# Performance work log

Measured on AMD Instinct MI355X. Metric: run time of the kernel, lower is better.

Reference implementation:

```python
import jax, jax.numpy as jnp
import numpy as np

N, C, T, V = 32, 64, 256, 25   # batch, channels, frames, joints
REL, OUT, K = 8, 64, 5         # rel_channels = C//8, out_channels, 5 topology branches
NU = 17                        # upper-body joints (lower = V - NU = 8)


def setup_inputs() -> dict:
    key = jax.random.key(0)
    ks = jax.random.split(key, 8)
    sC = np.float32(1.0 / np.sqrt(C))
    sR = np.float32(1.0 / np.sqrt(REL))
    return {
        "x": jax.random.normal(ks[0], (N, C, T, V), jnp.float32),
        "A": jax.random.uniform(ks[1], (K, V, V), jnp.float32),
        # stacked 1x1-conv weights for the 5 branches (conv{k}_1_1, _1_2, _2, _3, _4)
        "W11": jax.random.normal(ks[2], (K, REL, C), jnp.float32) * sC,
        "b11": jnp.zeros((K, REL), jnp.float32),
        "W12": jax.random.normal(ks[3], (K, REL, C), jnp.float32) * sC,
        "b12": jnp.zeros((K, REL), jnp.float32),
        "W2": jax.random.normal(ks[4], (K, REL, C), jnp.float32) * sC,
        "b2": jnp.zeros((K, REL), jnp.float32),
        "W3": jax.random.normal(ks[5], (K, OUT, C), jnp.float32) * sC,
        "b3": jnp.zeros((K, OUT), jnp.float32),
        "W4": jax.random.normal(ks[6], (K, OUT, REL), jnp.float32) * sR,
        "b4": jnp.zeros((K, OUT), jnp.float32),
    }


def reference(x, A, W11, b11, W12, b12, W2, b2, W3, b3, W4, b4):
    # 1x1 conv followed by mean over T commutes with the (linear) conv:
    # conv(x).mean(T) == W @ x.mean(T) + b. Pool once, reuse across branches.
    mu = jnp.mean(x[:, :, :, :NU], axis=2)   # (N, C, 17)
    ml = jnp.mean(x[:, :, :, NU:], axis=2)   # (N, C, 8)

    u11 = jnp.einsum('krc,ncv->knrv', W11, mu) + b11[:, None, :, None]  # (K,N,R,17)
    u2 = jnp.einsum('krc,ncv->knrv', W2, mu) + b2[:, None, :, None]     # (K,N,R,17)
    l12 = jnp.einsum('krc,ncv->knrv', W12, ml) + b12[:, None, :, None]  # (K,N,R,8)
    l2 = jnp.einsum('krc,ncv->knrv', W2, ml) + b2[:, None, :, None]     # (K,N,R,8)

    # pairwise-difference topology blocks
    x_a = jnp.tanh(u11[..., :, None] - u2[..., None, :])   # (K,N,R,17,17)
    x_b = jnp.tanh(u11[..., :, None] - l2[..., None, :])   # (K,N,R,17,8)
    x_c = jnp.tanh(l12[..., :, None] - u2[..., None, :])   # (K,N,R,8,17)
    x_d = jnp.tanh(l12[..., :, None] - l2[..., None, :])   # (K,N,R,8,8)

    up = jnp.concatenate([x_a, x_b], axis=-1)   # (K,N,R,17,25)
    lo = jnp.concatenate([x_c, x_d], axis=-1)   # (K,N,R,8,25)

    # the original rotates the upper blocks: branch k uses upper from branch (k+1)%5
    up_rot = jnp.concatenate([up[1:], up[:1]], axis=0)
    full = jnp.concatenate([up_rot, lo], axis=-2)  # (K,N,R,25,25)

    graphs = jnp.einsum('kor,knruv->knouv', W4, full) + b4[:, None, :, None, None]  # (K,N,O,25,25)

    alpha = jnp.ones((K,), jnp.float32)  # default branch scales
    g = graphs * alpha[:, None, None, None, None] + A[:, None, None, :, :]

    x2 = jnp.einsum('koc,nctv->knotv', W3, x) + b3[:, None, :, None, None]  # (K,N,O,T,25)
    out = jnp.einsum('knouv,knotv->notu', g, x2)  # summed over the 5 branches
    return out, graphs
```

## Files before the change

### kernel.cpp

```cpp
#include <hip/hip_runtime.h>
#include <cstdint>
#include <cstddef>

#define N_  32
#define C_  64
#define T_  256
#define V_  25
#define R_  8
#define O_  64
#define K_  5
#define NU_ 17
#define U_  25
#define CV  (C_ * V_)
#define OG  2
#define NB  (OG * 32)

#define OUT_ELEMS ((size_t)N_ * O_ * T_ * V_)

typedef __attribute__((ext_vector_type(8))) short bf16x8;
typedef __attribute__((ext_vector_type(4))) float f32x4;

static __device__ __forceinline__ unsigned short f2bf(float f) {
    union { float f; unsigned u; } c; c.f = f;
    return (unsigned short)((c.u + 0x8000u) >> 16);
}
static __device__ __forceinline__ float bf2f(unsigned short h) {
    union { unsigned u; float f; } c; c.u = ((unsigned)h) << 16; return c.f;
}
static __device__ __forceinline__ float bf_lo(unsigned d) {
    union { unsigned u; float f; } c; c.u = d << 16; return c.f;
}
static __device__ __forceinline__ float bf_hi(unsigned d) {
    union { unsigned u; float f; } c; c.u = d & 0xFFFF0000u; return c.f;
}
static __device__ __forceinline__ unsigned pk2(float a, float b) {
    union { float f; unsigned u; } ca, cb; ca.f = a; cb.f = b;
    return ((ca.u + 0x8000u) >> 16) | ((cb.u + 0x8000u) & 0xFFFF0000u);
}
static __device__ __forceinline__ unsigned cvtpk(float a, float b) {
    unsigned r;
    asm("v_cvt_pk_bf16_f32 %0, %1, %2" : "=v"(r) : "v"(a), "v"(b));
    return r;
}

__global__ void k_xcast(const float* __restrict__ x, unsigned short* __restrict__ xT3,
                        float* __restrict__ pp) {
    __shared__ unsigned short tile[C_][408];
    int bid = blockIdx.x;
    int n = bid >> 4, tb = bid & 15;
    int tid = threadIdx.x;
    const float* xb = x + (size_t)n * C_ * T_ * V_ + tb * 400;
#pragma unroll
    for (int it = 0; it < 25; ++it) {
        int i = it * 256 + tid;
        int c = i / 100, q = i - c * 100;
        float4 v4 = *(const float4*)(xb + (size_t)c * (T_ * V_) + q * 4);
        uint2 w;
        w.x = pk2(v4.x, v4.y);
        w.y = pk2(v4.z, v4.w);
        *(uint2*)&tile[c][q * 4] = w;
    }
    __syncthreads();
    unsigned short* dstb = xT3 + ((size_t)(n * 16 + tb) * 200) * 128;
    for (int i = tid; i < 200 * 16; i += 256) {
        int sp = i >> 4, tl = i & 15;
        int v = sp >> 3, c0 = (sp & 7) * 8;
        unsigned short h[8];
#pragma unroll
        for (int j = 0; j < 8; ++j) h[j] = tile[c0 + j][tl * 25 + v];
        uint4 pk;
        pk.x = (unsigned)h[0] | ((unsigned)h[1] << 16);
        pk.y = (unsigned)h[2] | ((unsigned)h[3] << 16);
        pk.z = (unsigned)h[4] | ((unsigned)h[5] << 16);
        pk.w = (unsigned)h[6] | ((unsigned)h[7] << 16);
        *(uint4*)(dstb + (size_t)sp * 128 + tl * 8) = pk;
    }
    float* ppd = pp + ((size_t)n * 16 + tb) * CV;
    for (int e = tid; e < CV; e += 256) {
        int c = e / 25, v = e - c * 25;
        float s = 0.f;
#pragma unroll
        for (int t = 0; t < 16; ++t) s += bf2f(tile[c][t * 25 + v]);
        ppd[e] = s;
    }
}

__global__ void k_pool(const float* __restrict__ x, float* __restrict__ pool) {
    int nc = blockIdx.x;
    int t  = threadIdx.x;
    const float* px = x + ((size_t)nc * T_ + t) * V_;
    float acc[V_];
#pragma unroll
    for (int v = 0; v < V_; ++v) acc[v] = px[v];
#pragma unroll
    for (int off = 32; off > 0; off >>= 1) {
#pragma unroll
        for (int v = 0; v < V_; ++v) acc[v] += __shfl_down(acc[v], off, 64);
    }
    __shared__ float sm[4][V_];
    int wave = t >> 6, lane = t & 63;
    if (lane == 0) {
#pragma unroll
        for (int v = 0; v < V_; ++v) sm[wave][v] = acc[v];
    }
    __syncthreads();
    if (t < V_) {
        float s = sm[0][t] + sm[1][t] + sm[2][t] + sm[3][t];
        pool[(size_t)nc * V_ + t] = s * (1.0f / T_);
    }
}

__global__ void k_tvals(const float* __restrict__ pool,
                        const float* __restrict__ W11, const float* __restrict__ b11,
                        const float* __restrict__ W12, const float* __restrict__ b12,
                        const float* __restrict__ W2,  const float* __restrict__ b2,
                        float* __restrict__ t2o, float* __restrict__ tSo) {
    int kn = blockIdx.x;
    int k = kn / N_, n = kn % N_;
    int tid = threadIdx.x;
    int r = tid >> 5, v = tid & 31;
    if (v >= V_) return;
    const float* pp = pool + (size_t)n * C_ * V_ + v;
    const float* w2 = W2 + ((size_t)k * R_ + r) * C_;
    const float* w1 = ((v < NU_) ? W11 : W12) + ((size_t)k * R_ + r) * C_;
    float a2 = b2[k * R_ + r];
    float a1 = (v < NU_) ? b11[k * R_ + r] : b12[k * R_ + r];
    for (int c = 0; c < C_; ++c) {
        float p = pp[(size_t)c * V_];
        a2 += w2[c] * p;
        a1 += w1[c] * p;
    }
    size_t idx = (((size_t)k * N_ + n) * R_ + r) * V_ + v;
    t2o[idx] = a2;
    tSo[idx] = a1;
}

__global__ void k_graphs(const float* __restrict__ t2v, const float* __restrict__ tSv,
                         const float* __restrict__ W4, const float* __restrict__ b4,
                         float* __restrict__ graphs) {
    int kn = blockIdx.x;
    int k = kn / N_, n = kn % N_;
    int kup = (k + 1) % K_;
    __shared__ float F[R_][V_ * V_];
    __shared__ float w4s[O_][R_];
    __shared__ float b4s[O_];
    int tid = threadIdx.x;
    for (int i = tid; i < O_ * R_; i += 256) w4s[i / R_][i % R_] = W4[(size_t)k * O_ * R_ + i];
    if (tid < O_) b4s[tid] = b4[k * O_ + tid];
    for (int idx = tid; idx < R_ * V_ * V_; idx += 256) {
        int r = idx / (V_ * V_), uv = idx % (V_ * V_);
        int u = uv / V_, v = uv % V_;
        int ks = (u < NU_) ? kup : k;
        size_t base = (((size_t)ks * N_ + n) * R_ + r) * V_;
        F[r][uv] = tanhf(tSv[base + u] - t2v[base + v]);
    }
    __syncthreads();
    float* gout = graphs + ((size_t)k * N_ + n) * O_ * (V_ * V_);
    for (int idx = tid; idx < O_ * V_ * V_; idx += 256) {
        int o = idx / (V_ * V_), uv = idx % (V_ * V_);
        float a = b4s[o];
#pragma unroll
        for (int r = 0; r < R_; ++r) a += w4s[o][r] * F[r][uv];
        gout[idx] = a;
    }
}

__global__ void k_graphs2c(const float* __restrict__ pp,
                           const float* __restrict__ W11, const float* __restrict__ b11,
                           const float* __restrict__ W12, const float* __restrict__ b12,
                           const float* __restrict__ W2,  const float* __restrict__ b2,
                           const float* __restrict__ W4,  const float* __restrict__ b4,
                           float* __restrict__ graphs) {
    int bid = blockIdx.x;
    int og = bid & 1;
    int kn = bid >> 1;
    int k = kn / N_, n = kn % N_;
    int kup = (k + 1) % K_;
    __shared__ float poolL[CV];
    __shared__ float t2s[2][R_][V_];
    __shared__ float tSs[2][R_][V_];
    __shared__ float F[R_][V_ * V_];
    __shared__ float w4s[O_][R_];
    __shared__ float b4s[O_];
    int tid = threadIdx.x;
    for (int i = tid; i < O_ * R_; i += 512) w4s[i / R_][i % R_] = W4[(size_t)k * O_ * R_ + i];
    if (tid < O_) b4s[tid] = b4[k * O_ + tid];
    const float* ppn = pp + (size_t)n * 16 * CV;
    for (int i = tid; i < CV; i += 512) {
        float s = 0.f;
#pragma unroll
        for (int tb = 0; tb < 16; ++tb) s += ppn[(size_t)tb * CV + i];
        poolL[i] = s * (1.0f / T_);
    }
    __syncthreads();
    for (int i = tid; i < 2 * R_ * V_; i += 512) {
        int ks = i / (R_ * V_);
        int rem = i - ks * (R_ * V_);
        int r = rem / V_, v = rem - r * V_;
        int kk = ks ? kup : k;
        const float* w2 = W2 + ((size_t)kk * R_ + r) * C_;
        const float* w1 = ((v < NU_) ? W11 : W12) + ((size_t)kk * R_ + r) * C_;
        float a2 = b2[kk * R_ + r];
        float a1 = (v < NU_) ? b11[kk * R_ + r] : b12[kk * R_ + r];
        for (int c = 0; c < C_; ++c) {
            float p = poolL[c * 25 + v];
            a2 += w2[c] * p;
            a1 += w1[c] * p;
        }
        t2s[ks][r][v] = a2;
        tSs[ks][r][v] = a1;
    }
    __syncthreads();
    for (int idx = tid; idx < R_ * V_ * V_; idx += 512) {
        int r = idx / (V_ * V_), uv = idx % (V_ * V_);
        int u = uv / V_, v = uv % V_;
        int ks = (u < NU_) ? 1 : 0;
        F[r][uv] = tanhf(tSs[ks][r][u] - t2s[ks][r][v]);
    }
    __syncthreads();
    float* gout = graphs + ((size_t)k * N_ + n) * O_ * (V_ * V_);
    const int half = O_ * V_ * V_ / 2;
    for (int idx = og * half + tid; idx < (og + 1) * half; idx += 512) {
        int o = idx / (V_ * V_), uv = idx % (V_ * V_);
        float a = b4s[o];
#pragma unroll
        for (int r = 0; r < R_; ++r) a += w4s[o][r] * F[r][uv];
        gout[idx] = a;
    }
}

__global__ __launch_bounds__(256, 4) void k_main_fast(
    const unsigned short* __restrict__ xT3,
    const float* __restrict__ graphs,
    const float* __restrict__ Adj,
    const float* __restrict__ W3,
    const float* __restrict__ b3,
    float* __restrict__ out) {

    __shared__ unsigned short Hs[2][4][NB][8];
    __shared__ f32x4 Gls4[OG * 625];
    __shared__ float Gls1[OG * 625];
    __shared__ unsigned short W3kmh[K_ * OG * C_];
    __shared__ float biasS[NB];

    const int tid = threadIdx.x;
    int bid = blockIdx.x;
    bid = (bid & 7) * 128 + (bid >> 3);
    const int obase = (bid & 31) * OG;
    const int n = bid >> 5;
    const int lane = tid & 63;
    const int wv_ = tid >> 6;

    const size_t kstride = (size_t)N_ * O_ * 625;
    for (int i = tid; i < OG * 625; i += 256) {
        int o = i / 625, uv = i - o * 625;
        int u = uv / 25, v = uv - u * 25;
        size_t gb = ((size_t)n * O_ + obase + o) * 625 + uv;
        f32x4 g4;
        g4[0] = graphs[gb]               + Adj[uv];
        g4[1] = graphs[gb + kstride]     + Adj[625 + uv];
        g4[2] = graphs[gb + 2 * kstride] + Adj[1250 + uv];
        g4[3] = graphs[gb + 3 * kstride] + Adj[1875 + uv];
        int idx = o * 625 + v * 25 + u;
        Gls4[idx] = g4;
        Gls1[idx] = graphs[gb + 4 * kstride] + Adj[2500 + uv];
    }
    for (int i = tid; i < K_ * OG * C_; i += 256) {
        int k = i / (OG * C_);
        int rem = i - k * (OG * C_);
        int o = rem >> 6, c = rem & 63;
        W3kmh[(k * OG + o) * C_ + c] = f2bf(W3[((size_t)k * O_ + obase + o) * C_ + c]);
    }
    __syncthreads();

    if (tid < NB) {
        int o = tid >> 5, u = tid & 31;
        float bv = 0.f;
        if (u < U_) {
            f32x4 s4 = {0.f, 0.f, 0.f, 0.f};
            float s5 = 0.f;
            for (int v = 0; v < V_; ++v) {
                int idx = o * 625 + v * 25 + u;
                s4 += Gls4[idx];
                s5 += Gls1[idx];
            }
            bv = s4[0] * b3[0 * O_ + obase + o] + s4[1] * b3[1 * O_ + obase + o]
               + s4[2] * b3[2 * O_ + obase + o] + s4[3] * b3[3 * O_ + obase + o]
               + s5 * b3[4 * O_ + obase + o];
        }
        biasS[tid] = bv;
    }

    const int sl = wv_;
    const int hncol = lane;
    const int ho = hncol >> 5;
    const int hu = hncol & 31;
    const f32x4* gp4 = &Gls4[ho * 625 + hu];
    const float* gp1 = &Gls1[ho * 625 + hu];
    const unsigned short* wbh = &W3kmh[ho * C_ + sl * 8];
    uint4* hw = (uint4*)&Hs[0][sl][hncol][0];

    auto h_form = [&](uint4* hwp, const int parOff , f32x4 g, float g5) {
        float gk[5] = {g[0], g[1], g[2], g[3], g5};
        float h0 = 0.f, h1 = 0.f, h2 = 0.f, h3 = 0.f;
        float h4 = 0.f, h5 = 0.f, h6 = 0.f, h7 = 0.f;
#pragma unroll
        for (int k = 0; k < K_; ++k) {
            uint4 wk = *(const uint4*)(wbh + parOff + k * (OG * C_));
            float gv_ = gk[k];
            h0 += bf_lo(wk.x) * gv_; h1 += bf_hi(wk.x) * gv_;
            h2 += bf_lo(wk.y) * gv_; h3 += bf_hi(wk.y) * gv_;
            h4 += bf_lo(wk.z) * gv_; h5 += bf_hi(wk.z) * gv_;
            h6 += bf_lo(wk.w) * gv_; h7 += bf_hi(wk.w) * gv_;
        }
        uint4 hv;
        hv.x = cvtpk(h0, h1); hv.y = cvtpk(h2, h3);
        hv.z = cvtpk(h4, h5); hv.w = cvtpk(h6, h7);
        *hwp = hv;
    };
    auto ld_g = [&](int voff25, f32x4& g, float& g5) {
        if (hu < U_) { g = gp4[voff25]; g5 = gp1[voff25]; }
        else { g = (f32x4){0.f, 0.f, 0.f, 0.f}; g5 = 0.f; }
    };

    const int wm = wv_;
    const int lr = lane & 15;
    const int eg = lane >> 4;

    f32x4 acc[4][4];
#pragma unroll
    for (int mt = 0; mt < 4; ++mt)
#pragma unroll
        for (int nt = 0; nt < 4; ++nt) acc[mt][nt] = (f32x4){0.f, 0.f, 0.f, 0.f};

    const unsigned short* An = xT3 + (size_t)n * (T_ * CV);
    const unsigned short* a0 = An + ((size_t)((wm * 4 + 0) * 200 + eg)) * 128 + lr * 8;
    const unsigned short* a1 = a0 + 200 * 128;
    const unsigned short* a2 = a0 + 400 * 128;
    const unsigned short* a3 = a0 + 600 * 128;
    const char* hrb = (const char*)&Hs[0][eg][lr][0];

    auto consume = [&](int sub , int bufb ) {
        uint4 av0 = *(const uint4*)(a0 + sub);
        uint4 av1 = *(const uint4*)(a1 + sub);
        uint4 av2 = *(const uint4*)(a2 + sub);
        uint4 av3 = *(const uint4*)(a3 + sub);
        bf16x8 b[4];
#pragma unroll
        for (int nt = 0; nt < 4; ++nt)
            b[nt] = *(const bf16x8*)(hrb + bufb + nt * 256);
        __builtin_amdgcn_s_setprio(1);
        union { uint4 u; bf16x8 h; } c0, c1, c2, c3;
        c0.u = av0; c1.u = av1; c2.u = av2; c3.u = av3;
#pragma unroll
        for (int nt = 0; nt < 4; ++nt) acc[0][nt] = __builtin_amdgcn_mfma_f32_16x16x32_bf16(c0.h, b[nt], acc[0][nt], 0, 0, 0);
#pragma unroll
        for (int nt = 0; nt < 4; ++nt) acc[1][nt] = __builtin_amdgcn_mfma_f32_16x16x32_bf16(c1.h, b[nt], acc[1][nt], 0, 0, 0);
#pragma unroll
        for (int nt = 0; nt < 4; ++nt) acc[2][nt] = __builtin_amdgcn_mfma_f32_16x16x32_bf16(c2.h, b[nt], acc[2][nt], 0, 0, 0);
#pragma unroll
        for (int nt = 0; nt < 4; ++nt) acc[3][nt] = __builtin_amdgcn_mfma_f32_16x16x32_bf16(c3.h, b[nt], acc[3][nt], 0, 0, 0);
        __builtin_amdgcn_s_setprio(0);
    };

    f32x4 gv; float gv5;
    ld_g(0, gv, gv5);
    h_form(hw, 0, gv, gv5);
    __syncthreads();

    for (int kc2 = 0; kc2 < 25; ++kc2) {
        consume(0, 0);
        h_form(hw + 256, 32, gv, gv5);
        __syncthreads();
        consume(512, 4096);
        if (kc2 + 1 < 25) {
            ld_g((kc2 + 1) * 25, gv, gv5);
            h_form(hw, 0, gv, gv5);
        }
        __syncthreads();
        a0 += 1024; a1 += 1024; a2 += 1024; a3 += 1024;
    }

#pragma unroll
    for (int nt = 0; nt < 4; ++nt) {
        int ncol = nt * 16 + lr;
        int ol = ncol >> 5;
        int u  = ncol & 31;
        if (u < U_) {
            float bv = biasS[ncol];
            float* ob = out + ((size_t)n * O_ + obase + ol) * T_ * V_ + u;
#pragma unroll
            for (int mt = 0; mt < 4; ++mt) {
                int t0 = wm * 64 + mt * 16 + eg * 4;
#pragma unroll
                for (int r2 = 0; r2 < 4; ++r2)
                    ob[(size_t)(t0 + r2) * V_] = acc[mt][nt][r2] + bv;
            }
        }
    }
}

#define OB 4
#define TB 64
__global__ __launch_bounds__(256, 1) void k_main_slow(
    const float* __restrict__ x, const float* __restrict__ graphs,
    const float* __restrict__ A, const float* __restrict__ W3,
    const float* __restrict__ b3, float* __restrict__ out) {
    int bid = blockIdx.x;
    int tb = bid & 3;
    int ob = (bid >> 2) & 15;
    int n  = bid >> 6;
    int tid = threadIdx.x;
    int ol = tid >> 6;
    int tl = tid & 63;
    int t = tb * TB + tl;
    int o = ob * OB + ol;

    __shared__ float Gs[K_][OB][V_][28];
    __shared__ float W3s[K_][OB][C_];
    __shared__ float b3s[K_][OB];

    for (int i = tid; i < K_ * OB * V_ * V_; i += 256) {
        int k   = i / (OB * V_ * V_);
        int rem = i % (OB * V_ * V_);
        int oo  = rem / (V_ * V_);
        int uv  = rem % (V_ * V_);
        Gs[k][oo][uv / V_][uv % V_] =
            graphs[(((size_t)k * N_ + n) * O_ + ob * OB + oo) * (V_ * V_) + uv]
            + A[k * V_ * V_ + uv];
    }
    for (int i = tid; i < K_ * OB * C_; i += 256) {
        int k   = i / (OB * C_);
        int rem = i % (OB * C_);
        int oo  = rem / C_, c = rem % C_;
        W3s[k][oo][c] = W3[((size_t)k * O_ + ob * OB + oo) * C_ + c];
    }
    if (tid < K_ * OB) b3s[tid / OB][tid % OB] = b3[(tid / OB) * O_ + ob * OB + tid % OB];
    __syncthreads();

    float x2[K_][V_];
#pragma unroll
    for (int k = 0; k < K_; ++k)
#pragma unroll
        for (int v = 0; v < V_; ++v) x2[k][v] = b3s[k][ol];

    const float* xb = x + ((size_t)n * C_ * T_ + t) * V_;
    for (int c = 0; c < C_; ++c) {
        const float* p = xb + (size_t)c * T_ * V_;
        float xv[V_];
#pragma unroll
        for (int v = 0; v < V_; ++v) xv[v] = p[v];
#pragma unroll
        for (int k = 0; k < K_; ++k) {
            float w = W3s[k][ol][c];
#pragma unroll
            for (int v = 0; v < V_; ++v) x2[k][v] += w * xv[v];
        }
    }

    float acc[V_];
#pragma unroll
    for (int u = 0; u < V_; ++u) acc[u] = 0.0f;
#pragma unroll
    for (int k = 0; k < K_; ++k) {
#pragma unroll
        for (int u = 0; u < V_; ++u) {
            const float* gr = &Gs[k][ol][u][0];
            float s = 0.0f;
#pragma unroll
            for (int v = 0; v < V_; ++v) s += gr[v] * x2[k][v];
            acc[u] += s;
        }
    }
    float* po = out + (((size_t)n * O_ + o) * T_ + t) * V_;
#pragma unroll
    for (int u = 0; u < V_; ++u) po[u] = acc[u];
}

extern "C" void kernel_launch(void* const* d_in, const int* in_sizes, int n_in,
                              void* d_out, int out_size, void* d_ws, size_t ws_size,
                              hipStream_t stream) {
    const float* x   = (const float*)d_in[0];
    const float* A   = (const float*)d_in[1];
    const float* W11 = (const float*)d_in[2];
    const float* b11 = (const float*)d_in[3];
    const float* W12 = (const float*)d_in[4];
    const float* b12 = (const float*)d_in[5];
    const float* W2  = (const float*)d_in[6];
    const float* b2  = (const float*)d_in[7];
    const float* W3  = (const float*)d_in[8];
    const float* b3  = (const float*)d_in[9];
    const float* W4  = (const float*)d_in[10];
    const float* b4  = (const float*)d_in[11];

    float* out    = (float*)d_out;
    float* graphs = out + OUT_ELEMS;

    const size_t xT_bytes = sizeof(unsigned short) * (size_t)N_ * T_ * CV;
    const size_t pp_bytes = sizeof(float) * (size_t)N_ * 16 * CV;
    const size_t hdr      = (size_t)(1 << 20);
    const bool fast = (ws_size >= hdr + xT_bytes + pp_bytes);

    const size_t poolElems = (size_t)N_ * C_ * V_;
    const size_t tElems    = (size_t)K_ * N_ * R_ * V_;
    const size_t slowNeed  = (poolElems + 2 * tElems) * sizeof(float);

    float* scratch = (fast || ws_size >= slowNeed) ? (float*)d_ws : out;
    float* pool = scratch;
    float* t2v  = scratch + poolElems;
    float* tSv  = t2v + tElems;
    unsigned short* xT3 = (unsigned short*)((char*)d_ws + hdr);
    float* pp = (float*)((char*)d_ws + hdr + xT_bytes);

    if (fast) {
        k_xcast   <<<N_ * 16, 256, 0, stream>>>(x, xT3, pp);
        k_graphs2c<<<K_ * N_ * 2, 512, 0, stream>>>(pp, W11, b11, W12, b12, W2, b2, W4, b4, graphs);
        k_main_fast<<<N_ * 32, 256, 0, stream>>>(xT3, graphs, A, W3, b3, out);
    } else {
        k_pool  <<<N_ * C_, 256, 0, stream>>>(x, pool);
        k_tvals <<<K_ * N_, 256, 0, stream>>>(pool, W11, b11, W12, b12, W2, b2, t2v, tSv);
        k_graphs<<<K_ * N_, 256, 0, stream>>>(t2v, tSv, W4, b4, graphs);
        k_main_slow<<<N_ * (O_ / OB) * 4, 256, 0, stream>>>(x, graphs, A, W3, b3, out);
    }
}
```

Before: 111.4 us.

## Double-buffer H tiles to drop a barrier and store graphs as bf16

```diff
diff --git a/kernel.cpp b/kernel.cpp
--- a/kernel.cpp
+++ b/kernel.cpp
@@ -237,9 +237,9 @@
     const float* __restrict__ b3,
     float* __restrict__ out) {
 
-    __shared__ unsigned short Hs[2][4][NB][8];
-    __shared__ f32x4 Gls4[OG * 625];
-    __shared__ float Gls1[OG * 625];
+    __shared__ unsigned short Hs[4][4][NB][8];
+    __shared__ uint2 Gbf4[OG * 625];
+    __shared__ unsigned short Gbf1[OG * 625];
     __shared__ unsigned short W3kmh[K_ * OG * C_];
     __shared__ float biasS[NB];
 
@@ -256,14 +256,15 @@
         int o = i / 625, uv = i - o * 625;
         int u = uv / 25, v = uv - u * 25;
         size_t gb = ((size_t)n * O_ + obase + o) * 625 + uv;
-        f32x4 g4;
-        g4[0] = graphs[gb]               + Adj[uv];
-        g4[1] = graphs[gb + kstride]     + Adj[625 + uv];
-        g4[2] = graphs[gb + 2 * kstride] + Adj[1250 + uv];
-        g4[3] = graphs[gb + 3 * kstride] + Adj[1875 + uv];
+        float g0 = graphs[gb]               + Adj[uv];
+        float g1 = graphs[gb + kstride]     + Adj[625 + uv];
+        float g2 = graphs[gb + 2 * kstride] + Adj[1250 + uv];
+        float g3 = graphs[gb + 3 * kstride] + Adj[1875 + uv];
+        float g4 = graphs[gb + 4 * kstride] + Adj[2500 + uv];
         int idx = o * 625 + v * 25 + u;
-        Gls4[idx] = g4;
-        Gls1[idx] = graphs[gb + 4 * kstride] + Adj[2500 + uv];
+        uint2 w; w.x = pk2(g0, g1); w.y = pk2(g2, g3);
+        Gbf4[idx] = w;
+        Gbf1[idx] = f2bf(g4);
     }
     for (int i = tid; i < K_ * OG * C_; i += 256) {
         int k = i / (OG * C_);
@@ -277,16 +278,17 @@
         int o = tid >> 5, u = tid & 31;
         float bv = 0.f;
         if (u < U_) {
-            f32x4 s4 = {0.f, 0.f, 0.f, 0.f};
-            float s5 = 0.f;
+            float s0 = 0.f, s1 = 0.f, s2 = 0.f, s3 = 0.f, s4 = 0.f;
             for (int v = 0; v < V_; ++v) {
                 int idx = o * 625 + v * 25 + u;
-                s4 += Gls4[idx];
-                s5 += Gls1[idx];
+                uint2 w = Gbf4[idx];
+                s0 += bf_lo(w.x); s1 += bf_hi(w.x);
+                s2 += bf_lo(w.y); s3 += bf_hi(w.y);
+                s4 += bf2f(Gbf1[idx]);
             }
-            bv = s4[0] * b3[0 * O_ + obase + o] + s4[1] * b3[1 * O_ + obase + o]
-               + s4[2] * b3[2 * O_ + obase + o] + s4[3] * b3[3 * O_ + obase + o]
-               + s5 * b3[4 * O_ + obase + o];
+            bv = s0 * b3[0 * O_ + obase + o] + s1 * b3[1 * O_ + obase + o]
+               + s2 * b3[2 * O_ + obase + o] + s3 * b3[3 * O_ + obase + o]
+               + s4 * b3[4 * O_ + obase + o];
         }
         biasS[tid] = bv;
     }
@@ -295,12 +297,12 @@
     const int hncol = lane;
     const int ho = hncol >> 5;
     const int hu = hncol & 31;
-    const f32x4* gp4 = &Gls4[ho * 625 + hu];
-    const float* gp1 = &Gls1[ho * 625 + hu];
+    const uint2* gp4 = &Gbf4[ho * 625 + hu];
+    const unsigned short* gp1 = &Gbf1[ho * 625 + hu];
     const unsigned short* wbh = &W3kmh[ho * C_ + sl * 8];
-    uint4* hw = (uint4*)&Hs[0][sl][hncol][0];
-
-    auto h_form = [&](uint4* hwp, const int parOff , f32x4 g, float g5) {
+    char* hwb = (char*)&Hs[0][sl][hncol][0];
+
+    auto h_form = [&](char* hwp, const int parOff , f32x4 g, float g5) {
         float gk[5] = {g[0], g[1], g[2], g[3], g5};
         float h0 = 0.f, h1 = 0.f, h2 = 0.f, h3 = 0.f;
         float h4 = 0.f, h5 = 0.f, h6 = 0.f, h7 = 0.f;
@@ -316,11 +318,15 @@
         uint4 hv;
         hv.x = cvtpk(h0, h1); hv.y = cvtpk(h2, h3);
         hv.z = cvtpk(h4, h5); hv.w = cvtpk(h6, h7);
-        *hwp = hv;
+        *(uint4*)hwp = hv;
     };
     auto ld_g = [&](int voff25, f32x4& g, float& g5) {
-        if (hu < U_) { g = gp4[voff25]; g5 = gp1[voff25]; }
-        else { g = (f32x4){0.f, 0.f, 0.f, 0.f}; g5 = 0.f; }
+        if (hu < U_) {
+            uint2 gw = gp4[voff25];
+            g[0] = bf_lo(gw.x); g[1] = bf_hi(gw.x);
+            g[2] = bf_lo(gw.y); g[3] = bf_hi(gw.y);
+            g5 = bf2f(gp1[voff25]);
+        } else { g = (f32x4){0.f, 0.f, 0.f, 0.f}; g5 = 0.f; }
     };
 
     const int wm = wv_;
@@ -365,17 +371,19 @@
 
     f32x4 gv; float gv5;
     ld_g(0, gv, gv5);
-    h_form(hw, 0, gv, gv5);
+    h_form(hwb, 0, gv, gv5);
+    h_form(hwb + 4096, 32, gv, gv5);
     __syncthreads();
 
     for (int kc2 = 0; kc2 < 25; ++kc2) {
-        consume(0, 0);
-        h_form(hw + 256, 32, gv, gv5);
-        __syncthreads();
-        consume(512, 4096);
+        const int rb = (kc2 & 1) * 8192;
+        const int wb = 8192 - rb;
+        if (kc2 + 1 < 25) ld_g((kc2 + 1) * 25, gv, gv5);
+        consume(0, rb);
+        consume(512, rb + 4096);
         if (kc2 + 1 < 25) {
-            ld_g((kc2 + 1) * 25, gv, gv5);
-            h_form(hw, 0, gv, gv5);
+            h_form(hwb + wb, 0, gv, gv5);
+            h_form(hwb + wb + 4096, 32, gv, gv5);
         }
         __syncthreads();
         a0 += 1024; a1 += 1024; a2 += 1024; a3 += 1024;
```

Result: no change. 109.4 us (-1.8%).
